# Kernel tuning notes

Measured on AMD Instinct MI355X. Metric: run time of the kernel, lower is better.

Reference implementation:

```python
import jax, jax.numpy as jnp
import numpy as np

EMBED_DIM = 256
NUM_HEADS = 8
HEAD_DIM = EMBED_DIM // NUM_HEADS
MAX_WAVELENGTH = 10000.0
ROPE_PERCENT = 0.5


def _p_rope(x, positions, head_dim, max_wavelength, rope_percent):
    # x: [BH, N, head_dim]; partial RoPE: rotate only first rope_percent of angle pairs
    half = head_dim // 2
    rope_angles = int(rope_percent * half)
    fraction = 2.0 * jnp.arange(rope_angles, dtype=jnp.float32) / head_dim
    timescale = max_wavelength ** fraction  # [rope_angles]
    sinusoid = positions[:, None] / timescale[None, :]  # [N, rope_angles]
    sin = jnp.sin(sinusoid).astype(x.dtype)
    cos = jnp.cos(sinusoid).astype(x.dtype)
    first, second = jnp.split(x, 2, axis=-1)  # each [BH, N, half]
    f_r, f_p = first[..., :rope_angles], first[..., rope_angles:]
    s_r, s_p = second[..., :rope_angles], second[..., rope_angles:]
    f_out = jnp.concatenate([f_r * cos - s_r * sin, f_p], axis=-1)
    s_out = jnp.concatenate([s_r * cos + f_r * sin, s_p], axis=-1)
    return jnp.concatenate([f_out, s_out], axis=-1)


def setup_inputs() -> dict:
    key = jax.random.key(0)
    ks = jax.random.split(key, 10)
    B, N, D = 2, 4096, EMBED_DIM
    s = 1.0 / np.sqrt(D)
    inp = {
        "hidden_states": jax.random.normal(ks[0], (B, N, D), jnp.float32),
        "q_w": jax.random.normal(ks[1], (D, D), jnp.float32) * s,
        "q_b": jnp.zeros((D,), jnp.float32),
        "k_w": jax.random.normal(ks[2], (D, D), jnp.float32) * s,
        "k_b": jnp.zeros((D,), jnp.float32),
        "v_w": jax.random.normal(ks[3], (D, D), jnp.float32) * s,
        "v_b": jnp.zeros((D,), jnp.float32),
        "o_w": jax.random.normal(ks[4], (D, D), jnp.float32) * s,
        "o_b": jnp.zeros((D,), jnp.float32),
        "attention_biases": jax.random.normal(ks[5], (NUM_HEADS, 2), jnp.float32) * 0.02,
        "num_channels": 8,
        "sequence_length": 512,
    }
    return inp


def reference(hidden_states, q_w, q_b, k_w, k_b, v_w, v_b, o_w, o_b,
              attention_biases, num_channels, sequence_length):
    B, N, D = hidden_states.shape
    H, hd = NUM_HEADS, HEAD_DIM
    scaling = hd ** -0.5

    def shape(t):  # [B,N,D] -> [B*H, N, hd]
        return t.reshape(B, N, H, hd).transpose(0, 2, 1, 3).reshape(B * H, N, hd)

    q = shape(hidden_states @ q_w.T + q_b) * scaling
    k = shape(hidden_states @ k_w.T + k_b)
    v = shape(hidden_states @ v_w.T + v_b)

    positions = jnp.arange(N, dtype=jnp.float32)
    k = _p_rope(k, positions, hd, MAX_WAVELENGTH, ROPE_PERCENT)
    q = _p_rope(q, positions, hd, MAX_WAVELENGTH, ROPE_PERCENT)

    attn = jnp.einsum('bqd,bkd->bqk', q, k).reshape(B, H, N, N)

    variate_ids = jnp.arange(N) // sequence_length
    same = (variate_ids[:, None] == variate_ids[None, :])  # [N,N] bool
    bias_same = attention_biases[:, 0][None, :, None, None]
    bias_diff = attention_biases[:, 1][None, :, None, None]
    attn = attn + jnp.where(same[None, None], bias_same, bias_diff)

    attn = jax.nn.softmax(attn, axis=-1).reshape(B * H, N, N)
    out = jnp.einsum('bqk,bkd->bqd', attn, v)  # [B*H, N, hd]
    out = out.reshape(B, H, N, hd).transpose(0, 2, 1, 3).reshape(B, N, D)
    return out @ o_w.T + o_b
```

## Files before the change

### kernel.cpp

```cpp
#include <hip/hip_runtime.h>
#include <cstdint>
#include <cstddef>

typedef __attribute__((ext_vector_type(8))) short bf16x8;
typedef __attribute__((ext_vector_type(4))) short short4v;
typedef __attribute__((ext_vector_type(4))) float f32x4;
typedef __attribute__((ext_vector_type(2))) unsigned int u32x2;
typedef __attribute__((ext_vector_type(4))) unsigned int u32x4;

extern "C" __device__ float __ocml_native_exp2_f32(float);
#define EXP2 __ocml_native_exp2_f32

__device__ __forceinline__ unsigned cvt_pk_bf16(float a, float b) {
  unsigned r;
  asm("v_cvt_pk_bf16_f32 %0, %1, %2" : "=v"(r) : "v"(a), "v"(b));
  return r;
}

__device__ __forceinline__ short f2bf(float f) {
  unsigned u = __float_as_uint(f);
  u += 0x7FFFu + ((u >> 16) & 1u);
  return (short)(u >> 16);
}

__constant__ float INV_TS[8] = {
  1.0f, 0.5623413251903491f, 0.31622776601683794f, 0.17782794100389228f,
  0.1f, 0.05623413251903491f, 0.031622776601683794f, 0.017782794100389228f
};

__global__ __launch_bounds__(256) void gemm_qkv_rope(
    const float* __restrict__ X,
    const float* __restrict__ W0, const float* __restrict__ W1, const float* __restrict__ W2,
    const float* __restrict__ b0, const float* __restrict__ b1, const float* __restrict__ b2,
    short* __restrict__ Qo, short* __restrict__ Ko, short* __restrict__ Vt)
{
  __shared__ short sA[128 * 40];
  __shared__ short sB[64 * 40];
  const int t = threadIdx.x;
  const int w = t >> 6, l = t & 63;
  const int l15 = l & 15, lg = l >> 4;
  const int rbase = blockIdx.x * 128;
  const int cgbase = blockIdx.y * 64;
  const int mat = cgbase >> 8;
  const float* W = (mat == 0) ? W0 : ((mat == 1) ? W1 : W2);
  const float* bias = (mat == 0) ? b0 : ((mat == 1) ? b1 : b2);
  const int wbase = cgbase & 255;

  const int ar = t >> 1, akc = (t & 1) * 16;
  const int br = t >> 2, bkc = (t & 3) * 8;

  const float* Bg = W + (size_t)(wbase + br) * 256 + bkc;
  const float* Agf = X + (size_t)(rbase + ar) * 256 + akc;

  const int wr = w >> 1, wc = w & 1;

  f32x4 acc[4][2];
#pragma unroll
  for (int i = 0; i < 4; ++i) {
    acc[i][0] = {0.f, 0.f, 0.f, 0.f};
    acc[i][1] = {0.f, 0.f, 0.f, 0.f};
  }

  for (int k0 = 0; k0 < 256; k0 += 32) {
    f32x4 a0 = *(const f32x4*)(Agf + k0);
    f32x4 a1 = *(const f32x4*)(Agf + k0 + 4);
    f32x4 a2 = *(const f32x4*)(Agf + k0 + 8);
    f32x4 a3 = *(const f32x4*)(Agf + k0 + 12);
    u32x4 pa0, pa1;
    pa0.x = cvt_pk_bf16(a0[0], a0[1]); pa0.y = cvt_pk_bf16(a0[2], a0[3]);
    pa0.z = cvt_pk_bf16(a1[0], a1[1]); pa0.w = cvt_pk_bf16(a1[2], a1[3]);
    pa1.x = cvt_pk_bf16(a2[0], a2[1]); pa1.y = cvt_pk_bf16(a2[2], a2[3]);
    pa1.z = cvt_pk_bf16(a3[0], a3[1]); pa1.w = cvt_pk_bf16(a3[2], a3[3]);
    f32x4 bv0 = *(const f32x4*)(Bg + k0);
    f32x4 bv1 = *(const f32x4*)(Bg + k0 + 4);
    u32x4 pb;
    pb.x = cvt_pk_bf16(bv0[0], bv0[1]); pb.y = cvt_pk_bf16(bv0[2], bv0[3]);
    pb.z = cvt_pk_bf16(bv1[0], bv1[1]); pb.w = cvt_pk_bf16(bv1[2], bv1[3]);

    __syncthreads();
    *(u32x4*)(sA + ar * 40 + akc)     = pa0;
    *(u32x4*)(sA + ar * 40 + akc + 8) = pa1;
    *(u32x4*)(sB + br * 40 + bkc)     = pb;
    __syncthreads();

    bf16x8 af[4], bfr[2];
#pragma unroll
    for (int i = 0; i < 4; ++i)
      af[i] = *(const bf16x8*)(sA + (wr * 64 + i * 16 + l15) * 40 + lg * 8);
#pragma unroll
    for (int j = 0; j < 2; ++j)
      bfr[j] = *(const bf16x8*)(sB + (wc * 32 + j * 16 + l15) * 40 + lg * 8);
#pragma unroll
    for (int i = 0; i < 4; ++i)
#pragma unroll
      for (int j = 0; j < 2; ++j)
        acc[i][j] = __builtin_amdgcn_mfma_f32_16x16x32_bf16(af[i], bfr[j], acc[i][j], 0, 0, 0);
  }

  const int cm = wbase + wc * 32;
  const int hh = cm >> 5;
  const float bv0 = bias[cm + l15];
  const float bv1 = bias[cm + 16 + l15];
  const float SCL_Q = 0.17677669529663687f * 1.4426950408889634f;

#pragma unroll
  for (int i = 0; i < 4; ++i) {
    const int m0 = rbase + wr * 64 + i * 16 + lg * 4;
    const int b = m0 >> 12, n0 = m0 & 4095;
    if (mat < 2) {
      short* dst = (mat == 0 ? Qo : Ko) + (size_t)(b * 8 + hh) * 131072 + (size_t)n0 * 32 + l15;
#pragma unroll
      for (int jj = 0; jj < 4; ++jj) {
        float v0 = acc[i][0][jj] + bv0;
        float v1 = acc[i][1][jj] + bv1;
        if (mat == 0) { v0 *= SCL_Q; v1 *= SCL_Q; }
        if (l15 < 8) {
          float ang = (float)(n0 + jj) * INV_TS[l15];
          float s = sinf(ang), c = cosf(ang);
          float r0 = v0 * c - v1 * s;
          float r1 = v1 * c + v0 * s;
          v0 = r0; v1 = r1;
        }
        dst[jj * 32]      = f2bf(v0);
        dst[jj * 32 + 16] = f2bf(v1);
      }
    } else {
      short* dstv = Vt + (size_t)(b * 8 + hh) * 131072 + n0;
#pragma unroll
      for (int j = 0; j < 2; ++j) {
        const float bv = j ? bv1 : bv0;
        short4v pk;
#pragma unroll
        for (int jj = 0; jj < 4; ++jj) pk[jj] = f2bf(acc[i][j][jj] + bv);
        *(short4v*)(dstv + (size_t)(j * 16 + l15) * 4096) = pk;
      }
    }
  }
}

__global__ __launch_bounds__(256, 4) void attn_fwd(
    const short* __restrict__ Qg, const short* __restrict__ Kg, const short* __restrict__ Vg,
    const float* __restrict__ ab, const int* __restrict__ slp,
    float* __restrict__ Op, float* __restrict__ denp)
{
  __shared__ short sK[2][64 * 40];
  __shared__ short sV[2][32 * 72];
  __shared__ short sP[4][16 * 72];
  const int t = threadIdx.x, w = t >> 6, l = t & 63;
  const int l15 = l & 15, lg = l >> 4;
  const int bh = blockIdx.y, h = bh & 7;
  const int z = blockIdx.z;
  const int qb = blockIdx.x * 128 + w * 32;
  const int sl = *slp;

  const short* Qb = Qg + (size_t)bh * (4096 * 32);
  const short* Kb = Kg + (size_t)bh * (4096 * 32);
  const short* Vb = Vg + (size_t)bh * (32 * 4096);

  bf16x8 qf[2];
  qf[0] = *(const bf16x8*)(Qb + (size_t)(qb + l15) * 32 + lg * 8);
  qf[1] = *(const bf16x8*)(Qb + (size_t)(qb + 16 + l15) * 32 + lg * 8);

  const float LOG2E = 1.4426950408889634f;
  const float lbs = ab[h * 2] * LOG2E, lbd = ab[h * 2 + 1] * LOG2E;
  const int qv[2]  = { (qb + l15) / sl, (qb + 16 + l15) / sl };
  const int qlo[2] = { qv[0] * sl, qv[1] * sl };

  short* P = &sP[w][0];
  short* pw = P + l15 * 72 + lg * 4;
  const short* pr = P + l15 * 72 + lg * 8;

  const f32x4 fz = {0.f, 0.f, 0.f, 0.f};
  f32x4 Oacc[2][2];
  Oacc[0][0] = fz; Oacc[0][1] = fz; Oacc[1][0] = fz; Oacc[1][1] = fz;
  float den[2] = {0.f, 0.f};

  const int kt0 = z * 32, kt1 = kt0 + 32;
  const int kstart = kt0 * 64;

  const int kr = t >> 2, kc0 = (t & 3) * 8;
  const int vd = t >> 3, vk0 = (t & 7) * 8;
  const short* kg = Kb + (size_t)(kstart + kr) * 32 + kc0;
  const short* vg = Vb + (size_t)vd * 4096 + kstart + vk0;

  bf16x8 krg = *(const bf16x8*)kg;
  bf16x8 vrg = *(const bf16x8*)vg;
  *(bf16x8*)(&sK[0][0] + kr * 40 + kc0) = krg;
  *(bf16x8*)(&sV[0][0] + vd * 72 + vk0) = vrg;
  kg += 64 * 32; vg += 64;
  krg = *(const bf16x8*)kg;
  vrg = *(const bf16x8*)vg;
  __syncthreads();

  int kv = kstart / sl;
  int rem = (kv + 1) * sl - kstart;
  int cur = 0;

#pragma unroll 2
  for (int kt = kt0; kt < kt1; ++kt) {
    *(bf16x8*)(&sK[cur ^ 1][0] + kr * 40 + kc0) = krg;
    *(bf16x8*)(&sV[cur ^ 1][0] + vd * 72 + vk0) = vrg;
    const int adv = (kt + 2 < kt1) ? 1 : 0;
    kg += adv * (64 * 32); vg += adv * 64;
    krg = *(const bf16x8*)kg;
    vrg = *(const bf16x8*)vg;

    const short* sKc = &sK[cur][0];
    const short* sVc = &sV[cur][0];

    f32x4 S[2][4];
#pragma unroll
    for (int t4 = 0; t4 < 4; ++t4) {
      bf16x8 kf = *(const bf16x8*)(sKc + (t4 * 16 + l15) * 40 + lg * 8);
      S[0][t4] = __builtin_amdgcn_mfma_f32_16x16x32_bf16(kf, qf[0], fz, 0, 0, 0);
      S[1][t4] = __builtin_amdgcn_mfma_f32_16x16x32_bf16(kf, qf[1], fz, 0, 0, 0);
    }

    const int kb0 = kt * 64;
    const bool uni = (rem >= 64);
    float lb[2];
    lb[0] = (qv[0] == kv) ? lbs : lbd;
    lb[1] = (qv[1] == kv) ? lbs : lbd;

#pragma unroll
    for (int g = 0; g < 2; ++g) {
      if (uni) {
#pragma unroll
        for (int t4 = 0; t4 < 4; ++t4) {
          float p0 = EXP2(S[g][t4][0] + lb[g]);
          float p1 = EXP2(S[g][t4][1] + lb[g]);
          float p2 = EXP2(S[g][t4][2] + lb[g]);
          float p3 = EXP2(S[g][t4][3] + lb[g]);
          den[g] += (p0 + p1) + (p2 + p3);
          u32x2 u; u.x = cvt_pk_bf16(p0, p1); u.y = cvt_pk_bf16(p2, p3);
          *(u32x2*)(pw + t4 * 16) = u;
        }
      } else {
#pragma unroll
        for (int t4 = 0; t4 < 4; ++t4) {
          const int gk = kb0 + t4 * 16 + lg * 4;
          float p[4];
#pragma unroll
          for (int j = 0; j < 4; ++j) {
            float lbj = ((unsigned)(gk + j - qlo[g]) < (unsigned)sl) ? lbs : lbd;
            p[j] = EXP2(S[g][t4][j] + lbj);
            den[g] += p[j];
          }
          u32x2 u; u.x = cvt_pk_bf16(p[0], p[1]); u.y = cvt_pk_bf16(p[2], p[3]);
          *(u32x2*)(pw + t4 * 16) = u;
        }
      }
#pragma unroll
      for (int kk = 0; kk < 2; ++kk) {
        bf16x8 pf = *(const bf16x8*)(pr + kk * 32);
        bf16x8 vf0 = *(const bf16x8*)(sVc + l15 * 72 + kk * 32 + lg * 8);
        bf16x8 vf1 = *(const bf16x8*)(sVc + (16 + l15) * 72 + kk * 32 + lg * 8);
        Oacc[g][0] = __builtin_amdgcn_mfma_f32_16x16x32_bf16(pf, vf0, Oacc[g][0], 0, 0, 0);
        Oacc[g][1] = __builtin_amdgcn_mfma_f32_16x16x32_bf16(pf, vf1, Oacc[g][1], 0, 0, 0);
      }
    }

    rem -= 64;
    while (rem <= 0) { kv += 1; rem += sl; }

    __syncthreads();
    cur ^= 1;
  }

#pragma unroll
  for (int g = 0; g < 2; ++g) {
    den[g] += __shfl_xor(den[g], 16, 64);
    den[g] += __shfl_xor(den[g], 32, 64);
  }

  const size_t zb = ((size_t)z * 16 + bh) * 4096;
  if (lg == 0) {
#pragma unroll
    for (int g = 0; g < 2; ++g)
      denp[zb + qb + g * 16 + l15] = den[g];
  }
#pragma unroll
  for (int g = 0; g < 2; ++g)
#pragma unroll
    for (int nt = 0; nt < 2; ++nt)
#pragma unroll
      for (int j = 0; j < 4; ++j) {
        const int n = qb + g * 16 + lg * 4 + j;
        Op[(zb + n) * 32 + nt * 16 + l15] = Oacc[g][nt][j];
      }
}

__global__ __launch_bounds__(256) void combine(
    const float* __restrict__ Op, const float* __restrict__ denp,
    short* __restrict__ attno)
{
  const int id = blockIdx.x * 256 + threadIdx.x;
  const int d4 = (id & 7) * 4;
  const int n  = (id >> 3) & 4095;
  const int bh = id >> 15;
  const size_t base = ((size_t)bh * 4096 + n) * 32 + d4;
  const size_t zoff = (size_t)16 * 4096 * 32;
  f32x4 o0 = *(const f32x4*)(Op + base);
  f32x4 o1 = *(const f32x4*)(Op + zoff + base);
  const float rd = 1.0f / (denp[bh * 4096 + n] + denp[16 * 4096 + bh * 4096 + n]);
  const int b = bh >> 3, hh = bh & 7;
  u32x2 u;
  u.x = cvt_pk_bf16((o0[0] + o1[0]) * rd, (o0[1] + o1[1]) * rd);
  u.y = cvt_pk_bf16((o0[2] + o1[2]) * rd, (o0[3] + o1[3]) * rd);
  *(u32x2*)(attno + ((size_t)(b * 4096 + n) * 256 + hh * 32 + d4)) = u;
}

template<int A_BF16, int OUT_BF16>
__global__ __launch_bounds__(256) void gemm_mfma(
    const void* __restrict__ Ain,
    const float* __restrict__ W0, const float* __restrict__ W1, const float* __restrict__ W2,
    const float* __restrict__ b0, const float* __restrict__ b1, const float* __restrict__ b2,
    void* __restrict__ Cout, int Ntot)
{
  __shared__ short sA[128 * 40];
  __shared__ short sB[64 * 40];
  const int t = threadIdx.x;
  const int w = t >> 6, l = t & 63;
  const int l15 = l & 15, lg = l >> 4;
  const int rbase = blockIdx.x * 128;
  const int cgbase = blockIdx.y * 64;
  const int mat = cgbase >> 8;
  const float* W = (mat == 0) ? W0 : ((mat == 1) ? W1 : W2);
  const float* bias = (mat == 0) ? b0 : ((mat == 1) ? b1 : b2);
  const int wbase = cgbase & 255;

  const int ar = t >> 1, akc = (t & 1) * 16;
  const int br = t >> 2, bkc = (t & 3) * 8;

  const float* Bg = W + (size_t)(wbase + br) * 256 + bkc;
  const float* Agf = (const float*)Ain + (size_t)(rbase + ar) * 256 + akc;
  const short* Agh = (const short*)Ain + (size_t)(rbase + ar) * 256 + akc;

  const int wr = w >> 1, wc = w & 1;

  f32x4 acc[4][2];
#pragma unroll
  for (int i = 0; i < 4; ++i) {
    acc[i][0] = {0.f, 0.f, 0.f, 0.f};
    acc[i][1] = {0.f, 0.f, 0.f, 0.f};
  }

  for (int k0 = 0; k0 < 256; k0 += 32) {
    u32x4 pa0, pa1;
    if constexpr (A_BF16) {
      pa0 = *(const u32x4*)(Agh + k0);
      pa1 = *(const u32x4*)(Agh + k0 + 8);
    } else {
      f32x4 a0 = *(const f32x4*)(Agf + k0);
      f32x4 a1 = *(const f32x4*)(Agf + k0 + 4);
      f32x4 a2 = *(const f32x4*)(Agf + k0 + 8);
      f32x4 a3 = *(const f32x4*)(Agf + k0 + 12);
      pa0.x = cvt_pk_bf16(a0[0], a0[1]); pa0.y = cvt_pk_bf16(a0[2], a0[3]);
      pa0.z = cvt_pk_bf16(a1[0], a1[1]); pa0.w = cvt_pk_bf16(a1[2], a1[3]);
      pa1.x = cvt_pk_bf16(a2[0], a2[1]); pa1.y = cvt_pk_bf16(a2[2], a2[3]);
      pa1.z = cvt_pk_bf16(a3[0], a3[1]); pa1.w = cvt_pk_bf16(a3[2], a3[3]);
    }
    f32x4 bv0 = *(const f32x4*)(Bg + k0);
    f32x4 bv1 = *(const f32x4*)(Bg + k0 + 4);
    u32x4 pb;
    pb.x = cvt_pk_bf16(bv0[0], bv0[1]); pb.y = cvt_pk_bf16(bv0[2], bv0[3]);
    pb.z = cvt_pk_bf16(bv1[0], bv1[1]); pb.w = cvt_pk_bf16(bv1[2], bv1[3]);

    __syncthreads();
    *(u32x4*)(sA + ar * 40 + akc)     = pa0;
    *(u32x4*)(sA + ar * 40 + akc + 8) = pa1;
    *(u32x4*)(sB + br * 40 + bkc)     = pb;
    __syncthreads();

    bf16x8 af[4], bfr[2];
#pragma unroll
    for (int i = 0; i < 4; ++i)
      af[i] = *(const bf16x8*)(sA + (wr * 64 + i * 16 + l15) * 40 + lg * 8);
#pragma unroll
    for (int j = 0; j < 2; ++j)
      bfr[j] = *(const bf16x8*)(sB + (wc * 32 + j * 16 + l15) * 40 + lg * 8);
#pragma unroll
    for (int i = 0; i < 4; ++i)
#pragma unroll
      for (int j = 0; j < 2; ++j)
        acc[i][j] = __builtin_amdgcn_mfma_f32_16x16x32_bf16(af[i], bfr[j], acc[i][j], 0, 0, 0);
  }

#pragma unroll
  for (int i = 0; i < 4; ++i)
#pragma unroll
    for (int j = 0; j < 2; ++j) {
      const int n = cgbase + wc * 32 + j * 16 + l15;
      const float bv = bias[wbase + wc * 32 + j * 16 + l15];
#pragma unroll
      for (int jj = 0; jj < 4; ++jj) {
        const size_t m = (size_t)(rbase + wr * 64 + i * 16 + lg * 4 + jj);
        const float val = acc[i][j][jj] + bv;
        if constexpr (OUT_BF16) ((short*)Cout)[m * Ntot + n] = f2bf(val);
        else                    ((float*)Cout)[m * Ntot + n] = val;
      }
    }
}

extern "C" void kernel_launch(void* const* d_in, const int* in_sizes, int n_in,
                              void* d_out, int out_size, void* d_ws, size_t ws_size,
                              hipStream_t stream) {
  (void)in_sizes; (void)n_in; (void)out_size; (void)ws_size;
  const float* hs = (const float*)d_in[0];
  const float* qw = (const float*)d_in[1];
  const float* qb = (const float*)d_in[2];
  const float* kw = (const float*)d_in[3];
  const float* kb = (const float*)d_in[4];
  const float* vw = (const float*)d_in[5];
  const float* vb = (const float*)d_in[6];
  const float* ow = (const float*)d_in[7];
  const float* ob = (const float*)d_in[8];
  const float* ab = (const float*)d_in[9];
  const int* sl   = (const int*)d_in[11];
  float* out = (float*)d_out;

  char* ws = (char*)d_ws;
  float* Op   = (float*)(ws);
  short* Qbf  = (short*)(ws + 16777216);
  short* Kbf  = (short*)(ws + 20971520);
  short* Vtb  = (short*)(ws + 25165824);
  float* denp = (float*)(ws + 29360128);
  short* attno= (short*)(ws + 29884416);

  gemm_qkv_rope<<<dim3(64, 12), 256, 0, stream>>>(hs, qw, kw, vw, qb, kb, vb, Qbf, Kbf, Vtb);
  attn_fwd<<<dim3(32, 16, 2), 256, 0, stream>>>(Qbf, Kbf, Vtb, ab, sl, Op, denp);
  combine<<<dim3(2048), 256, 0, stream>>>(Op, denp, attno);
  gemm_mfma<1, 0><<<dim3(64, 4), 256, 0, stream>>>(attno, ow, ow, ow, ob, ob, ob, out, 256);
}
```

Before: 94.41 us.

## Software-pipeline PV MFMA of second query group across iterations

```diff
diff --git a/kernel.cpp b/kernel.cpp
--- a/kernel.cpp
+++ b/kernel.cpp
@@ -145,7 +145,7 @@
 {
   __shared__ short sK[2][64 * 40];
   __shared__ short sV[2][32 * 72];
-  __shared__ short sP[4][16 * 72];
+  __shared__ short sP[4][2][16 * 72];
   const int t = threadIdx.x, w = t >> 6, l = t & 63;
   const int l15 = l & 15, lg = l >> 4;
   const int bh = blockIdx.y, h = bh & 7;
@@ -166,9 +166,10 @@
   const int qv[2]  = { (qb + l15) / sl, (qb + 16 + l15) / sl };
   const int qlo[2] = { qv[0] * sl, qv[1] * sl };
 
-  short* P = &sP[w][0];
-  short* pw = P + l15 * 72 + lg * 4;
-  const short* pr = P + l15 * 72 + lg * 8;
+  short* P0 = &sP[w][0][0];
+  short* P1 = &sP[w][1][0];
+  const int pwo = l15 * 72 + lg * 4;
+  const int pro = l15 * 72 + lg * 8;
 
   const f32x4 fz = {0.f, 0.f, 0.f, 0.f};
   f32x4 Oacc[2][2];
@@ -196,6 +197,12 @@
   int rem = (kv + 1) * sl - kstart;
   int cur = 0;
 
+  bf16x8 vprev[2][2];
+#pragma unroll
+  for (int kk = 0; kk < 2; ++kk)
+#pragma unroll
+    for (int nt = 0; nt < 2; ++nt) vprev[kk][nt] = bf16x8{0,0,0,0,0,0,0,0};
+
 #pragma unroll 2
   for (int kt = kt0; kt < kt1; ++kt) {
     *(bf16x8*)(&sK[cur ^ 1][0] + kr * 40 + kc0) = krg;
@@ -216,48 +223,86 @@
       S[1][t4] = __builtin_amdgcn_mfma_f32_16x16x32_bf16(kf, qf[1], fz, 0, 0, 0);
     }
 
+    if (kt > kt0) {
+#pragma unroll
+      for (int kk = 0; kk < 2; ++kk) {
+        bf16x8 pf = *(const bf16x8*)(P1 + pro + kk * 32);
+        Oacc[1][0] = __builtin_amdgcn_mfma_f32_16x16x32_bf16(pf, vprev[kk][0], Oacc[1][0], 0, 0, 0);
+        Oacc[1][1] = __builtin_amdgcn_mfma_f32_16x16x32_bf16(pf, vprev[kk][1], Oacc[1][1], 0, 0, 0);
+      }
+    }
+
     const int kb0 = kt * 64;
     const bool uni = (rem >= 64);
-    float lb[2];
-    lb[0] = (qv[0] == kv) ? lbs : lbd;
-    lb[1] = (qv[1] == kv) ? lbs : lbd;
-
-#pragma unroll
-    for (int g = 0; g < 2; ++g) {
-      if (uni) {
-#pragma unroll
-        for (int t4 = 0; t4 < 4; ++t4) {
-          float p0 = EXP2(S[g][t4][0] + lb[g]);
-          float p1 = EXP2(S[g][t4][1] + lb[g]);
-          float p2 = EXP2(S[g][t4][2] + lb[g]);
-          float p3 = EXP2(S[g][t4][3] + lb[g]);
-          den[g] += (p0 + p1) + (p2 + p3);
-          u32x2 u; u.x = cvt_pk_bf16(p0, p1); u.y = cvt_pk_bf16(p2, p3);
-          *(u32x2*)(pw + t4 * 16) = u;
+    const float lb0 = (qv[0] == kv) ? lbs : lbd;
+    const float lb1 = (qv[1] == kv) ? lbs : lbd;
+
+    if (uni) {
+#pragma unroll
+      for (int t4 = 0; t4 < 4; ++t4) {
+        float p0 = EXP2(S[0][t4][0] + lb0);
+        float p1 = EXP2(S[0][t4][1] + lb0);
+        float p2 = EXP2(S[0][t4][2] + lb0);
+        float p3 = EXP2(S[0][t4][3] + lb0);
+        den[0] += (p0 + p1) + (p2 + p3);
+        u32x2 u; u.x = cvt_pk_bf16(p0, p1); u.y = cvt_pk_bf16(p2, p3);
+        *(u32x2*)(P0 + pwo + t4 * 16) = u;
+      }
+    } else {
+#pragma unroll
+      for (int t4 = 0; t4 < 4; ++t4) {
+        const int gk = kb0 + t4 * 16 + lg * 4;
+        float p[4];
+#pragma unroll
+        for (int j = 0; j < 4; ++j) {
+          float lbj = ((unsigned)(gk + j - qlo[0]) < (unsigned)sl) ? lbs : lbd;
+          p[j] = EXP2(S[0][t4][j] + lbj);
+          den[0] += p[j];
         }
-      } else {
-#pragma unroll
-        for (int t4 = 0; t4 < 4; ++t4) {
-          const int gk = kb0 + t4 * 16 + lg * 4;
-          float p[4];
-#pragma unroll
-          for (int j = 0; j < 4; ++j) {
-            float lbj = ((unsigned)(gk + j - qlo[g]) < (unsigned)sl) ? lbs : lbd;
-            p[j] = EXP2(S[g][t4][j] + lbj);
-            den[g] += p[j];
-          }
-          u32x2 u; u.x = cvt_pk_bf16(p[0], p[1]); u.y = cvt_pk_bf16(p[2], p[3]);
-          *(u32x2*)(pw + t4 * 16) = u;
+        u32x2 u; u.x = cvt_pk_bf16(p[0], p[1]); u.y = cvt_pk_bf16(p[2], p[3]);
+        *(u32x2*)(P0 + pwo + t4 * 16) = u;
+      }
+    }
+
+    bf16x8 vcur[2][2];
+#pragma unroll
+    for (int kk = 0; kk < 2; ++kk)
+#pragma unroll
+      for (int nt = 0; nt < 2; ++nt)
+        vcur[kk][nt] = *(const bf16x8*)(sVc + (nt * 16 + l15) * 72 + kk * 32 + lg * 8);
+
+    if (uni) {
+#pragma unroll
+      for (int t4 = 0; t4 < 4; ++t4) {
+        float p0 = EXP2(S[1][t4][0] + lb1);
+        float p1 = EXP2(S[1][t4][1] + lb1);
+        float p2 = EXP2(S[1][t4][2] + lb1);
+        float p3 = EXP2(S[1][t4][3] + lb1);
+        den[1] += (p0 + p1) + (p2 + p3);
+        u32x2 u; u.x = cvt_pk_bf16(p0, p1); u.y = cvt_pk_bf16(p2, p3);
+        *(u32x2*)(P1 + pwo + t4 * 16) = u;
+      }
+    } else {
+#pragma unroll
+      for (int t4 = 0; t4 < 4; ++t4) {
+        const int gk = kb0 + t4 * 16 + lg * 4;
+        float p[4];
+#pragma unroll
+        for (int j = 0; j < 4; ++j) {
+          float lbj = ((unsigned)(gk + j - qlo[1]) < (unsigned)sl) ? lbs : lbd;
+          p[j] = EXP2(S[1][t4][j] + lbj);
+          den[1] += p[j];
         }
-      }
-#pragma unroll
-      for (int kk = 0; kk < 2; ++kk) {
-        bf16x8 pf = *(const bf16x8*)(pr + kk * 32);
-        bf16x8 vf0 = *(const bf16x8*)(sVc + l15 * 72 + kk * 32 + lg * 8);
-        bf16x8 vf1 = *(const bf16x8*)(sVc + (16 + l15) * 72 + kk * 32 + lg * 8);
-        Oacc[g][0] = __builtin_amdgcn_mfma_f32_16x16x32_bf16(pf, vf0, Oacc[g][0], 0, 0, 0);
-        Oacc[g][1] = __builtin_amdgcn_mfma_f32_16x16x32_bf16(pf, vf1, Oacc[g][1], 0, 0, 0);
-      }
+        u32x2 u; u.x = cvt_pk_bf16(p[0], p[1]); u.y = cvt_pk_bf16(p[2], p[3]);
+        *(u32x2*)(P1 + pwo + t4 * 16) = u;
+      }
+    }
+
+#pragma unroll
+    for (int kk = 0; kk < 2; ++kk) {
+      bf16x8 pf = *(const bf16x8*)(P0 + pro + kk * 32);
+      Oacc[0][0] = __builtin_amdgcn_mfma_f32_16x16x32_bf16(pf, vcur[kk][0], Oacc[0][0], 0, 0, 0);
+      Oacc[0][1] = __builtin_amdgcn_mfma_f32_16x16x32_bf16(pf, vcur[kk][1], Oacc[0][1], 0, 0, 0);
     }
 
     rem -= 64;
@@ -265,6 +310,17 @@
 
     __syncthreads();
     cur ^= 1;
+#pragma unroll
+    for (int kk = 0; kk < 2; ++kk)
+#pragma unroll
+      for (int nt = 0; nt < 2; ++nt) vprev[kk][nt] = vcur[kk][nt];
+  }
+
+#pragma unroll
+  for (int kk = 0; kk < 2; ++kk) {
+    bf16x8 pf = *(const bf16x8*)(P1 + pro + kk * 32);
+    Oacc[1][0] = __builtin_amdgcn_mfma_f32_16x16x32_bf16(pf, vprev[kk][0], Oacc[1][0], 0, 0, 0);
+    Oacc[1][1] = __builtin_amdgcn_mfma_f32_16x16x32_bf16(pf, vprev[kk][1], Oacc[1][1], 0, 0, 0);
   }
 
 #pragma unroll
```

Measured after the change: 93.47 us. No clear change (-1.0%).
